# Optimization experiments

Hardware: AMD Instinct MI355X
Metric: run time of the kernel (lower is better)

## Reference

```python
import jax, jax.numpy as jnp
import numpy as np

N_NODES = 50000
N_EDGES = 800000
D_IN, D_HID, D_OUT = 128, 128, 64


def setup_inputs() -> dict:
    key = jax.random.key(0)
    ks = jax.random.split(key, 10)
    return {
        "x": jax.random.normal(ks[0], (N_NODES, D_IN), dtype=jnp.float32),
        "edge_row": jax.random.randint(ks[1], (N_EDGES,), 0, N_NODES, dtype=jnp.int32),
        "edge_col": jax.random.randint(ks[2], (N_EDGES,), 0, N_NODES, dtype=jnp.int32),
        "edge_val": jax.random.uniform(ks[3], (N_EDGES,), dtype=jnp.float32),
        "W1": jax.random.normal(ks[4], (D_IN, D_HID), dtype=jnp.float32) * (1.0 / np.sqrt(D_HID)),
        "b1": jax.random.normal(ks[5], (D_HID,), dtype=jnp.float32) * (1.0 / np.sqrt(D_HID)),
        "W2": jax.random.normal(ks[6], (D_HID, D_HID), dtype=jnp.float32) * (1.0 / np.sqrt(D_HID)),
        "b2": jax.random.normal(ks[7], (D_HID,), dtype=jnp.float32) * (1.0 / np.sqrt(D_HID)),
        "W3": jax.random.normal(ks[8], (D_HID, D_OUT), dtype=jnp.float32) * (1.0 / np.sqrt(D_OUT)),
        "b3": jax.random.normal(ks[9], (D_OUT,), dtype=jnp.float32) * (1.0 / np.sqrt(D_OUT)),
    }


def _gcn_layer(x, edge_row, edge_col, edge_val, W, b):
    # support = x @ W          : dense GEMM [N, d_out]
    support = x @ W
    # spmm(adj, support)[i] = sum_e with row[e]==i: val[e] * support[col[e]]
    gathered = support[edge_col] * edge_val[:, None]  # [E, d_out]
    agg = jax.ops.segment_sum(gathered, edge_row, num_segments=x.shape[0])
    return agg + b


def reference(x, edge_row, edge_col, edge_val, W1, b1, W2, b2, W3, b3):
    # Layer 1 + ReLU (dropout is identity in eval)
    h = jax.nn.relu(_gcn_layer(x, edge_row, edge_col, edge_val, W1, b1))
    # Layer 2 + ReLU
    h = jax.nn.relu(_gcn_layer(h, edge_row, edge_col, edge_val, W2, b2))
    # Layer 3 (no activation)
    return _gcn_layer(h, edge_row, edge_col, edge_val, W3, b3)
```

## Files before the change

### kernel.cpp

```cpp
#include <hip/hip_runtime.h>

#define N_NODES 50000
#define N_EDGES 800000
#define SCAN_TILE 2048
#define CNT_STRIDE 16
#define GEMM1_BLOCKS 768
#define FUSED_BLOCKS 512
#define HIST_BLOCKS ((N_EDGES + 255) / 256)

static_assert(N_NODES < 65536, "col must fit in 16 bits for packed CSR");

typedef __attribute__((ext_vector_type(4))) float f32x4;
typedef __attribute__((ext_vector_type(8))) short bf16x8;

__device__ inline unsigned short f32_to_bf16(float f) {
    unsigned int u = __builtin_bit_cast(unsigned int, f);
    u += 0x7FFF + ((u >> 16) & 1);
    return (unsigned short)(u >> 16);
}
__device__ inline float bf16_to_f32(unsigned short h) {
    unsigned int u = ((unsigned int)h) << 16;
    return __builtin_bit_cast(float, u);
}

#define W128  (128 * 128)
#define W64   (128 * 64)
#define CNT4  (N_NODES * CNT_STRIDE / 4)

__global__ void zero_cnt(int* __restrict__ cnt) {
    int i = blockIdx.x * blockDim.x + threadIdx.x;
    if (i < CNT4) {
        int4 z = {0, 0, 0, 0};
        reinterpret_cast<int4*>(cnt)[i] = z;
    }
}

__global__ void hist_wt(const int* __restrict__ erow, int* __restrict__ cnt,
                        int* __restrict__ rank, const float* __restrict__ W1,
                        const float* __restrict__ W2, const float* __restrict__ W3,
                        unsigned short* __restrict__ Wt1,
                        unsigned short* __restrict__ Wt2,
                        unsigned short* __restrict__ Wt3) {
    if (blockIdx.x < HIST_BLOCKS) {
        int e = blockIdx.x * blockDim.x + threadIdx.x;
        if (e < N_EDGES) rank[e] = atomicAdd(&cnt[(size_t)erow[e] * CNT_STRIDE], 1);
        return;
    }
    long long r = (long long)(blockIdx.x - HIST_BLOCKS) * blockDim.x + threadIdx.x;
    if (r < W128) {
        int k = (int)r / 128, m = (int)r % 128;
        Wt1[m * 128 + k] = f32_to_bf16(W1[r]);
        return;
    }
    r -= W128;
    if (r < W128) {
        int k = (int)r / 128, m = (int)r % 128;
        Wt2[m * 128 + k] = f32_to_bf16(W2[r]);
        return;
    }
    r -= W128;
    if (r < W64) {
        int k = (int)r / 64, m = (int)r % 64;
        Wt3[m * 128 + k] = f32_to_bf16(W3[r]);
    }
}

__global__ void scan_fused(const int* __restrict__ cnt, int* __restrict__ tsum,
                           int* __restrict__ done, int* __restrict__ rptr,
                           int n, int ntiles) {
    __shared__ int sums[256];
    __shared__ int off_s;
    const int t = threadIdx.x;
    const int b = blockIdx.x;
    const int base = b * SCAN_TILE + t * 8;
    int v[8], pref[8];
    int s = 0;
#pragma unroll
    for (int i = 0; i < 8; ++i) {
        v[i] = (base + i < n) ? cnt[(size_t)(base + i) * CNT_STRIDE] : 0;
        s += v[i];
    }
    sums[t] = s;
    __syncthreads();
    for (int off = 1; off < 256; off <<= 1) {
        int x = (t >= off) ? sums[t - off] : 0;
        __syncthreads();
        sums[t] += x;
        __syncthreads();
    }
    int run = sums[t] - s;
#pragma unroll
    for (int i = 0; i < 8; ++i) {
        pref[i] = run;
        run += v[i];
    }
    if (t == 255) {
        tsum[b] = run;
        __threadfence();
        atomicAdd(done, 1);
    }
    if (t == 0) {
        while (__hip_atomic_load(done, __ATOMIC_ACQUIRE, __HIP_MEMORY_SCOPE_AGENT) <
               ntiles) {
        }
        __threadfence();
        int off = 0;
        for (int i = 0; i < b; ++i) off += tsum[i];
        off_s = off;
        if (b == 0) {
            int tot = 0;
            for (int i = 0; i < ntiles; ++i) tot += tsum[i];
            rptr[n] = tot;
        }
    }
    __syncthreads();
    const int off = off_s;
#pragma unroll
    for (int i = 0; i < 8; ++i) {
        int idx = base + i;
        if (idx < n) rptr[idx] = pref[i] + off;
    }
}

template <int NOUT>
__device__ __forceinline__ void mfma_phase(const unsigned short* Xs,
                                           const unsigned short* Ws,
                                           unsigned short* __restrict__ Yb,
                                           int block_row, int N) {
    constexpr int KP = 128 + 8;
    constexpr int NT = NOUT / 16;
    const int tid = threadIdx.x;
    const int wave = tid >> 6;
    const int lane = tid & 63;
    const int m = lane & 15;
    const int quad = lane >> 4;
    const int rowbase = wave * 16;

    f32x4 acc[NT];
#pragma unroll
    for (int t = 0; t < NT; ++t) acc[t] = (f32x4){0.f, 0.f, 0.f, 0.f};

#pragma unroll
    for (int kt = 0; kt < 4; ++kt) {
        bf16x8 a = *reinterpret_cast<const bf16x8*>(
            Xs + (rowbase + m) * KP + kt * 32 + quad * 8);
#pragma unroll
        for (int t = 0; t < NT; ++t) {
            bf16x8 b = *reinterpret_cast<const bf16x8*>(
                Ws + (t * 16 + m) * KP + kt * 32 + quad * 8);
            acc[t] = __builtin_amdgcn_mfma_f32_16x16x32_bf16(a, b, acc[t], 0, 0, 0);
        }
    }

#pragma unroll
    for (int t = 0; t < NT; ++t) {
#pragma unroll
        for (int r = 0; r < 4; ++r) {
            int grow = block_row + rowbase + quad * 4 + r;
            if (grow < N)
                Yb[(size_t)grow * NOUT + t * 16 + m] = f32_to_bf16(acc[t][r]);
        }
    }
}

template <int NOUT>
__device__ __forceinline__ void mfma_phase512(const unsigned short* Xs,
                                              const unsigned short* Ws,
                                              unsigned short* __restrict__ Yb,
                                              int block_row, int N) {
    constexpr int KP = 128 + 8;
    constexpr int NT = NOUT / 16;
    constexpr int NTH = NT / 2;
    const int tid = threadIdx.x;
    const int wave = tid >> 6;
    const int lane = tid & 63;
    const int m = lane & 15;
    const int quad = lane >> 4;
    const int rowbase = (wave & 3) * 16;
    const int tbase = (wave >> 2) * NTH;

    f32x4 acc[NTH];
#pragma unroll
    for (int t = 0; t < NTH; ++t) acc[t] = (f32x4){0.f, 0.f, 0.f, 0.f};

#pragma unroll
    for (int kt = 0; kt < 4; ++kt) {
        bf16x8 a = *reinterpret_cast<const bf16x8*>(
            Xs + (rowbase + m) * KP + kt * 32 + quad * 8);
#pragma unroll
        for (int t = 0; t < NTH; ++t) {
            bf16x8 b = *reinterpret_cast<const bf16x8*>(
                Ws + ((tbase + t) * 16 + m) * KP + kt * 32 + quad * 8);
            acc[t] = __builtin_amdgcn_mfma_f32_16x16x32_bf16(a, b, acc[t], 0, 0, 0);
        }
    }

#pragma unroll
    for (int t = 0; t < NTH; ++t) {
#pragma unroll
        for (int r = 0; r < 4; ++r) {
            int grow = block_row + rowbase + quad * 4 + r;
            if (grow < N)
                Yb[(size_t)grow * NOUT + (tbase + t) * 16 + m] = f32_to_bf16(acc[t][r]);
        }
    }
}

__global__ __launch_bounds__(256) void gemm1_fill(
    const float* __restrict__ x, const unsigned short* __restrict__ Wt,
    unsigned short* __restrict__ Yb, int N, int ntiles,
    const int* __restrict__ erow, const int* __restrict__ ecol,
    const float* __restrict__ eval, const int* __restrict__ rptr,
    const int* __restrict__ rank, unsigned int* __restrict__ cpack) {
    constexpr int KP = 128 + 8;
    __shared__ unsigned short Xs[64 * KP];
    __shared__ unsigned short Ws[128 * KP];
    const int tid = threadIdx.x;

    if (blockIdx.x >= GEMM1_BLOCKS) {
        int e = (blockIdx.x - GEMM1_BLOCKS) * blockDim.x + tid;
        if (e < N_EDGES) {
            int slot = rptr[erow[e]] + rank[e];
            unsigned int p = (unsigned int)(ecol[e] & 0xFFFF) |
                             ((unsigned int)f32_to_bf16(eval[e]) << 16);
            cpack[slot] = p;
        }
        return;
    }

    for (int idx = tid; idx < 128 * 16; idx += 256) {
        int r = idx >> 4, ch = idx & 15;
        uint4 v = *reinterpret_cast<const uint4*>(Wt + r * 128 + ch * 8);
        *reinterpret_cast<uint4*>(Ws + r * KP + ch * 8) = v;
    }

    for (int tile = blockIdx.x; tile < ntiles; tile += GEMM1_BLOCKS) {
        const int block_row = tile * 64;
        for (int idx = tid; idx < 64 * 16; idx += 256) {
            int r = idx >> 4, ch = idx & 15;
            int gr = block_row + r;
            if (gr >= N) gr = N - 1;
            const float4* xp =
                reinterpret_cast<const float4*>(x + (size_t)gr * 128 + ch * 8);
            float4 a = xp[0], b = xp[1];
            uint4 o;
            o.x = (unsigned int)f32_to_bf16(a.x) | ((unsigned int)f32_to_bf16(a.y) << 16);
            o.y = (unsigned int)f32_to_bf16(a.z) | ((unsigned int)f32_to_bf16(a.w) << 16);
            o.z = (unsigned int)f32_to_bf16(b.x) | ((unsigned int)f32_to_bf16(b.y) << 16);
            o.w = (unsigned int)f32_to_bf16(b.z) | ((unsigned int)f32_to_bf16(b.w) << 16);
            *reinterpret_cast<uint4*>(Xs + r * KP + ch * 8) = o;
        }
        __syncthreads();
        mfma_phase<128>(Xs, Ws, Yb, block_row, N);
        __syncthreads();
    }
}

template <int NOUT>
__global__ __launch_bounds__(512, 4) void gemm_fused_agg(
    const unsigned short* __restrict__ S,
    const int* __restrict__ rptr, const unsigned int* __restrict__ cpack,
    const float* __restrict__ bias,
    const unsigned short* __restrict__ Wt,
    unsigned short* __restrict__ Yb,
    int N, int ntiles) {
    constexpr int KP = 128 + 8;
    __shared__ unsigned short Xs[64 * KP];
    __shared__ unsigned short Ws[NOUT * KP];
    const int tid = threadIdx.x;
    const int group = tid >> 4;
    const int f8 = tid & 15;

    for (int idx = tid; idx < NOUT * 16; idx += 512) {
        int r = idx >> 4, ch = idx & 15;
        uint4 v = *reinterpret_cast<const uint4*>(Wt + r * 128 + ch * 8);
        *reinterpret_cast<uint4*>(Ws + r * KP + ch * 8) = v;
    }

    float bv[8];
#pragma unroll
    for (int i = 0; i < 8; ++i) bv[i] = bias[f8 * 8 + i];

    for (int tile = blockIdx.x; tile < ntiles; tile += gridDim.x) {
        const int block_row = tile * 64;
#pragma unroll
        for (int r4 = 0; r4 < 2; ++r4) {
            const int row = r4 * 32 + group;
            const int node = block_row + row;
            float acc[8];
#pragma unroll
            for (int i = 0; i < 8; ++i) acc[i] = bv[i];
            if (node < N) {
                const int beg = rptr[node];
                const int end = rptr[node + 1];
                int j = beg;
                for (; j + 8 <= end; j += 8) {
                    unsigned int p[8];
                    uint4 s[8];
#pragma unroll
                    for (int u = 0; u < 8; ++u) p[u] = cpack[j + u];
#pragma unroll
                    for (int u = 0; u < 8; ++u)
                        s[u] = *reinterpret_cast<const uint4*>(
                            S + (size_t)(p[u] & 0xFFFF) * 128 + f8 * 8);
#pragma unroll
                    for (int u = 0; u < 8; ++u) {
                        const float v = bf16_to_f32((unsigned short)(p[u] >> 16));
                        const unsigned short* sp =
                            reinterpret_cast<const unsigned short*>(&s[u]);
#pragma unroll
                        for (int i = 0; i < 8; ++i)
                            acc[i] = fmaf(v, bf16_to_f32(sp[i]), acc[i]);
                    }
                }
                if (j + 4 <= end) {
                    unsigned int p[4];
                    uint4 s[4];
#pragma unroll
                    for (int u = 0; u < 4; ++u) p[u] = cpack[j + u];
#pragma unroll
                    for (int u = 0; u < 4; ++u)
                        s[u] = *reinterpret_cast<const uint4*>(
                            S + (size_t)(p[u] & 0xFFFF) * 128 + f8 * 8);
#pragma unroll
                    for (int u = 0; u < 4; ++u) {
                        const float v = bf16_to_f32((unsigned short)(p[u] >> 16));
                        const unsigned short* sp =
                            reinterpret_cast<const unsigned short*>(&s[u]);
#pragma unroll
                        for (int i = 0; i < 8; ++i)
                            acc[i] = fmaf(v, bf16_to_f32(sp[i]), acc[i]);
                    }
                    j += 4;
                }
                if (j + 2 <= end) {
                    unsigned int p[2];
                    uint4 s[2];
#pragma unroll
                    for (int u = 0; u < 2; ++u) p[u] = cpack[j + u];
#pragma unroll
                    for (int u = 0; u < 2; ++u)
                        s[u] = *reinterpret_cast<const uint4*>(
                            S + (size_t)(p[u] & 0xFFFF) * 128 + f8 * 8);
#pragma unroll
                    for (int u = 0; u < 2; ++u) {
                        const float v = bf16_to_f32((unsigned short)(p[u] >> 16));
                        const unsigned short* sp =
                            reinterpret_cast<const unsigned short*>(&s[u]);
#pragma unroll
                        for (int i = 0; i < 8; ++i)
                            acc[i] = fmaf(v, bf16_to_f32(sp[i]), acc[i]);
                    }
                    j += 2;
                }
                if (j < end) {
                    unsigned int p = cpack[j];
                    uint4 s = *reinterpret_cast<const uint4*>(
                        S + (size_t)(p & 0xFFFF) * 128 + f8 * 8);
                    const float v = bf16_to_f32((unsigned short)(p >> 16));
                    const unsigned short* sp =
                        reinterpret_cast<const unsigned short*>(&s);
#pragma unroll
                    for (int i = 0; i < 8; ++i)
                        acc[i] = fmaf(v, bf16_to_f32(sp[i]), acc[i]);
                }
            }
            uint4 o;
            o.x = (unsigned int)f32_to_bf16(fmaxf(acc[0], 0.f)) |
                  ((unsigned int)f32_to_bf16(fmaxf(acc[1], 0.f)) << 16);
            o.y = (unsigned int)f32_to_bf16(fmaxf(acc[2], 0.f)) |
                  ((unsigned int)f32_to_bf16(fmaxf(acc[3], 0.f)) << 16);
            o.z = (unsigned int)f32_to_bf16(fmaxf(acc[4], 0.f)) |
                  ((unsigned int)f32_to_bf16(fmaxf(acc[5], 0.f)) << 16);
            o.w = (unsigned int)f32_to_bf16(fmaxf(acc[6], 0.f)) |
                  ((unsigned int)f32_to_bf16(fmaxf(acc[7], 0.f)) << 16);
            *reinterpret_cast<uint4*>(Xs + row * KP + f8 * 8) = o;
        }
        __syncthreads();
        mfma_phase512<NOUT>(Xs, Ws, Yb, block_row, N);
        __syncthreads();
    }
}

__global__ void aggregate_bf16_64(const unsigned short* __restrict__ S,
                                  const int* __restrict__ rptr,
                                  const unsigned int* __restrict__ cpack,
                                  const float* __restrict__ bias,
                                  float* __restrict__ out, int N) {
    const int node = blockIdx.x * (blockDim.x / 16) + threadIdx.x / 16;
    const int f4 = threadIdx.x & 15;
    if (node >= N) return;
    const int beg = rptr[node];
    const int end = rptr[node + 1];
    float acc[4];
#pragma unroll
    for (int i = 0; i < 4; ++i) acc[i] = bias[f4 * 4 + i];
    int j = beg;
    for (; j + 8 <= end; j += 8) {
        unsigned int p[8];
        uint2 s[8];
#pragma unroll
        for (int u = 0; u < 8; ++u) p[u] = cpack[j + u];
#pragma unroll
        for (int u = 0; u < 8; ++u)
            s[u] = *reinterpret_cast<const uint2*>(S + (size_t)(p[u] & 0xFFFF) * 64 + f4 * 4);
#pragma unroll
        for (int u = 0; u < 8; ++u) {
            const float v = bf16_to_f32((unsigned short)(p[u] >> 16));
            const unsigned short* sp = reinterpret_cast<const unsigned short*>(&s[u]);
#pragma unroll
            for (int i = 0; i < 4; ++i) acc[i] = fmaf(v, bf16_to_f32(sp[i]), acc[i]);
        }
    }
    if (j + 4 <= end) {
        unsigned int p[4];
        uint2 s[4];
#pragma unroll
        for (int u = 0; u < 4; ++u) p[u] = cpack[j + u];
#pragma unroll
        for (int u = 0; u < 4; ++u)
            s[u] = *reinterpret_cast<const uint2*>(S + (size_t)(p[u] & 0xFFFF) * 64 + f4 * 4);
#pragma unroll
        for (int u = 0; u < 4; ++u) {
            const float v = bf16_to_f32((unsigned short)(p[u] >> 16));
            const unsigned short* sp = reinterpret_cast<const unsigned short*>(&s[u]);
#pragma unroll
            for (int i = 0; i < 4; ++i) acc[i] = fmaf(v, bf16_to_f32(sp[i]), acc[i]);
        }
        j += 4;
    }
    if (j + 2 <= end) {
        unsigned int p[2];
        uint2 s[2];
#pragma unroll
        for (int u = 0; u < 2; ++u) p[u] = cpack[j + u];
#pragma unroll
        for (int u = 0; u < 2; ++u)
            s[u] = *reinterpret_cast<const uint2*>(S + (size_t)(p[u] & 0xFFFF) * 64 + f4 * 4);
#pragma unroll
        for (int u = 0; u < 2; ++u) {
            const float v = bf16_to_f32((unsigned short)(p[u] >> 16));
            const unsigned short* sp = reinterpret_cast<const unsigned short*>(&s[u]);
#pragma unroll
            for (int i = 0; i < 4; ++i) acc[i] = fmaf(v, bf16_to_f32(sp[i]), acc[i]);
        }
        j += 2;
    }
    if (j < end) {
        unsigned int p = cpack[j];
        uint2 s = *reinterpret_cast<const uint2*>(S + (size_t)(p & 0xFFFF) * 64 + f4 * 4);
        const float v = bf16_to_f32((unsigned short)(p >> 16));
        const unsigned short* sp = reinterpret_cast<const unsigned short*>(&s);
#pragma unroll
        for (int i = 0; i < 4; ++i) acc[i] = fmaf(v, bf16_to_f32(sp[i]), acc[i]);
    }
    float4 o = {acc[0], acc[1], acc[2], acc[3]};
    *reinterpret_cast<float4*>(out + (size_t)node * 64 + f4 * 4) = o;
}

extern "C" void kernel_launch(void* const* d_in, const int* in_sizes, int n_in,
                              void* d_out, int out_size, void* d_ws, size_t ws_size,
                              hipStream_t stream) {
    const float* x    = (const float*)d_in[0];
    const int*   erow = (const int*)d_in[1];
    const int*   ecol = (const int*)d_in[2];
    const float* eval = (const float*)d_in[3];
    const float* W1   = (const float*)d_in[4];
    const float* b1   = (const float*)d_in[5];
    const float* W2   = (const float*)d_in[6];
    const float* b2   = (const float*)d_in[7];
    const float* W3   = (const float*)d_in[8];
    const float* b3   = (const float*)d_in[9];
    float* out = (float*)d_out;

    const size_t nf = (size_t)N_NODES * 128;
    unsigned short* SA  = (unsigned short*)d_ws;
    unsigned short* SB  = SA + nf;
    unsigned short* Wt1 = SB + nf;
    unsigned short* Wt2 = Wt1 + 128 * 128;
    unsigned short* Wt3 = Wt2 + 128 * 128;
    int*   cnt    = (int*)(Wt3 + 64 * 128);
    int*   rank   = cnt + (size_t)N_NODES * CNT_STRIDE;
    int*   rptr   = rank + N_EDGES;
    unsigned int* cpack = (unsigned int*)(rptr + N_NODES + 1);
    int*   stsum  = (int*)(cpack + N_EDGES);
    int*   done   = cnt + 1;

    const int blk = 256;
    const int ntiles_g = (N_NODES + 63) / 64;
    const int agg_grid = (int)(((long long)N_NODES * 16 + blk - 1) / blk);
    const int ntiles = (N_NODES + SCAN_TILE - 1) / SCAN_TILE;
    const int wt_blocks = (W128 + W128 + W64 + blk - 1) / blk;

    zero_cnt<<<(CNT4 + blk - 1) / blk, blk, 0, stream>>>(cnt);
    hist_wt<<<HIST_BLOCKS + wt_blocks, blk, 0, stream>>>(erow, cnt, rank, W1, W2, W3,
                                                         Wt1, Wt2, Wt3);
    scan_fused<<<ntiles, 256, 0, stream>>>(cnt, stsum, done, rptr, N_NODES, ntiles);

    gemm1_fill<<<GEMM1_BLOCKS + HIST_BLOCKS, 256, 0, stream>>>(
        x, Wt1, SA, N_NODES, ntiles_g, erow, ecol, eval, rptr, rank, cpack);

    gemm_fused_agg<128><<<FUSED_BLOCKS, 512, 0, stream>>>(
        SA, rptr, cpack, b1, Wt2, SB, N_NODES, ntiles_g);

    gemm_fused_agg<64><<<FUSED_BLOCKS, 512, 0, stream>>>(
        SB, rptr, cpack, b2, Wt3, SA, N_NODES, ntiles_g);

    aggregate_bf16_64<<<agg_grid, blk, 0, stream>>>(SA, rptr, cpack, b3, out, N_NODES);
}
```

Baseline: 233.3 us.

## Overlap edge histogram with layer-1 GEMM and move CSR fill to own kernel

Merges the count-zeroing and weight transpose/convert into one prep kernel, then runs the edge histogram (atomic rank assignment) in the same launch as the layer-1 GEMM instead of in a separate kernel. The CSR packing step, which previously shared a launch with the GEMM, becomes its own small kernel after the scan. The launch count stays the same, but the GEMM now overlaps the atomic-heavy histogram rather than the lighter scatter fill. A risk is that the atomics contend with the GEMM's memory traffic.

```diff
diff --git a/kernel.cpp b/kernel.cpp
--- a/kernel.cpp
+++ b/kernel.cpp
@@ -27,26 +27,18 @@
 #define W64   (128 * 64)
 #define CNT4  (N_NODES * CNT_STRIDE / 4)
 
-__global__ void zero_cnt(int* __restrict__ cnt) {
-    int i = blockIdx.x * blockDim.x + threadIdx.x;
-    if (i < CNT4) {
+__global__ void prep(int* __restrict__ cnt, const float* __restrict__ W1,
+                     const float* __restrict__ W2, const float* __restrict__ W3,
+                     unsigned short* __restrict__ Wt1,
+                     unsigned short* __restrict__ Wt2,
+                     unsigned short* __restrict__ Wt3) {
+    long long r = (long long)blockIdx.x * blockDim.x + threadIdx.x;
+    if (r < CNT4) {
         int4 z = {0, 0, 0, 0};
-        reinterpret_cast<int4*>(cnt)[i] = z;
-    }
-}
-
-__global__ void hist_wt(const int* __restrict__ erow, int* __restrict__ cnt,
-                        int* __restrict__ rank, const float* __restrict__ W1,
-                        const float* __restrict__ W2, const float* __restrict__ W3,
-                        unsigned short* __restrict__ Wt1,
-                        unsigned short* __restrict__ Wt2,
-                        unsigned short* __restrict__ Wt3) {
-    if (blockIdx.x < HIST_BLOCKS) {
-        int e = blockIdx.x * blockDim.x + threadIdx.x;
-        if (e < N_EDGES) rank[e] = atomicAdd(&cnt[(size_t)erow[e] * CNT_STRIDE], 1);
+        reinterpret_cast<int4*>(cnt)[r] = z;
         return;
     }
-    long long r = (long long)(blockIdx.x - HIST_BLOCKS) * blockDim.x + threadIdx.x;
+    r -= CNT4;
     if (r < W128) {
         int k = (int)r / 128, m = (int)r % 128;
         Wt1[m * 128 + k] = f32_to_bf16(W1[r]);
@@ -62,63 +54,6 @@
     if (r < W64) {
         int k = (int)r / 64, m = (int)r % 64;
         Wt3[m * 128 + k] = f32_to_bf16(W3[r]);
-    }
-}
-
-__global__ void scan_fused(const int* __restrict__ cnt, int* __restrict__ tsum,
-                           int* __restrict__ done, int* __restrict__ rptr,
-                           int n, int ntiles) {
-    __shared__ int sums[256];
-    __shared__ int off_s;
-    const int t = threadIdx.x;
-    const int b = blockIdx.x;
-    const int base = b * SCAN_TILE + t * 8;
-    int v[8], pref[8];
-    int s = 0;
-#pragma unroll
-    for (int i = 0; i < 8; ++i) {
-        v[i] = (base + i < n) ? cnt[(size_t)(base + i) * CNT_STRIDE] : 0;
-        s += v[i];
-    }
-    sums[t] = s;
-    __syncthreads();
-    for (int off = 1; off < 256; off <<= 1) {
-        int x = (t >= off) ? sums[t - off] : 0;
-        __syncthreads();
-        sums[t] += x;
-        __syncthreads();
-    }
-    int run = sums[t] - s;
-#pragma unroll
-    for (int i = 0; i < 8; ++i) {
-        pref[i] = run;
-        run += v[i];
-    }
-    if (t == 255) {
-        tsum[b] = run;
-        __threadfence();
-        atomicAdd(done, 1);
-    }
-    if (t == 0) {
-        while (__hip_atomic_load(done, __ATOMIC_ACQUIRE, __HIP_MEMORY_SCOPE_AGENT) <
-               ntiles) {
-        }
-        __threadfence();
-        int off = 0;
-        for (int i = 0; i < b; ++i) off += tsum[i];
-        off_s = off;
-        if (b == 0) {
-            int tot = 0;
-            for (int i = 0; i < ntiles; ++i) tot += tsum[i];
-            rptr[n] = tot;
-        }
-    }
-    __syncthreads();
-    const int off = off_s;
-#pragma unroll
-    for (int i = 0; i < 8; ++i) {
-        int idx = base + i;
-        if (idx < n) rptr[idx] = pref[i] + off;
     }
 }
 
@@ -161,6 +96,118 @@
                 Yb[(size_t)grow * NOUT + t * 16 + m] = f32_to_bf16(acc[t][r]);
         }
     }
+}
+
+__global__ __launch_bounds__(256) void gemm1_hist(
+    const float* __restrict__ x, const unsigned short* __restrict__ Wt,
+    unsigned short* __restrict__ Yb, int N, int ntiles,
+    const int* __restrict__ erow, int* __restrict__ cnt, int* __restrict__ rank) {
+    constexpr int KP = 128 + 8;
+    __shared__ unsigned short Xs[64 * KP];
+    __shared__ unsigned short Ws[128 * KP];
+    const int tid = threadIdx.x;
+
+    if (blockIdx.x >= GEMM1_BLOCKS) {
+        int e = (blockIdx.x - GEMM1_BLOCKS) * blockDim.x + tid;
+        if (e < N_EDGES) rank[e] = atomicAdd(&cnt[(size_t)erow[e] * CNT_STRIDE], 1);
+        return;
+    }
+
+    for (int idx = tid; idx < 128 * 16; idx += 256) {
+        int r = idx >> 4, ch = idx & 15;
+        uint4 v = *reinterpret_cast<const uint4*>(Wt + r * 128 + ch * 8);
+        *reinterpret_cast<uint4*>(Ws + r * KP + ch * 8) = v;
+    }
+
+    for (int tile = blockIdx.x; tile < ntiles; tile += GEMM1_BLOCKS) {
+        const int block_row = tile * 64;
+        for (int idx = tid; idx < 64 * 16; idx += 256) {
+            int r = idx >> 4, ch = idx & 15;
+            int gr = block_row + r;
+            if (gr >= N) gr = N - 1;
+            const float4* xp =
+                reinterpret_cast<const float4*>(x + (size_t)gr * 128 + ch * 8);
+            float4 a = xp[0], b = xp[1];
+            uint4 o;
+            o.x = (unsigned int)f32_to_bf16(a.x) | ((unsigned int)f32_to_bf16(a.y) << 16);
+            o.y = (unsigned int)f32_to_bf16(a.z) | ((unsigned int)f32_to_bf16(a.w) << 16);
+            o.z = (unsigned int)f32_to_bf16(b.x) | ((unsigned int)f32_to_bf16(b.y) << 16);
+            o.w = (unsigned int)f32_to_bf16(b.z) | ((unsigned int)f32_to_bf16(b.w) << 16);
+            *reinterpret_cast<uint4*>(Xs + r * KP + ch * 8) = o;
+        }
+        __syncthreads();
+        mfma_phase<128>(Xs, Ws, Yb, block_row, N);
+        __syncthreads();
+    }
+}
+
+__global__ void scan_fused(const int* __restrict__ cnt, int* __restrict__ tsum,
+                           int* __restrict__ done, int* __restrict__ rptr,
+                           int n, int ntiles) {
+    __shared__ int sums[256];
+    __shared__ int off_s;
+    const int t = threadIdx.x;
+    const int b = blockIdx.x;
+    const int base = b * SCAN_TILE + t * 8;
+    int v[8], pref[8];
+    int s = 0;
+#pragma unroll
+    for (int i = 0; i < 8; ++i) {
+        v[i] = (base + i < n) ? cnt[(size_t)(base + i) * CNT_STRIDE] : 0;
+        s += v[i];
+    }
+    sums[t] = s;
+    __syncthreads();
+    for (int off = 1; off < 256; off <<= 1) {
+        int x = (t >= off) ? sums[t - off] : 0;
+        __syncthreads();
+        sums[t] += x;
+        __syncthreads();
+    }
+    int run = sums[t] - s;
+#pragma unroll
+    for (int i = 0; i < 8; ++i) {
+        pref[i] = run;
+        run += v[i];
+    }
+    if (t == 255) {
+        tsum[b] = run;
+        __threadfence();
+        atomicAdd(done, 1);
+    }
+    if (t == 0) {
+        while (__hip_atomic_load(done, __ATOMIC_ACQUIRE, __HIP_MEMORY_SCOPE_AGENT) <
+               ntiles) {
+        }
+        __threadfence();
+        int off = 0;
+        for (int i = 0; i < b; ++i) off += tsum[i];
+        off_s = off;
+        if (b == 0) {
+            int tot = 0;
+            for (int i = 0; i < ntiles; ++i) tot += tsum[i];
+            rptr[n] = tot;
+        }
+    }
+    __syncthreads();
+    const int off = off_s;
+#pragma unroll
+    for (int i = 0; i < 8; ++i) {
+        int idx = base + i;
+        if (idx < n) rptr[idx] = pref[i] + off;
+    }
+}
+
+__global__ void fill_csr(const int* __restrict__ erow, const int* __restrict__ ecol,
+                         const float* __restrict__ eval, const int* __restrict__ rptr,
+                         const int* __restrict__ rank,
+                         unsigned int* __restrict__ cpack) {
+    int e = blockIdx.x * blockDim.x + threadIdx.x;
+    if (e >= N_EDGES) return;
+    int slot = rptr[erow[e]] + rank[e];
+    unsigned int p = (unsigned int)(ecol[e] & 0xFFFF) |
+                     ((unsigned int)f32_to_bf16(eval[e]) << 16);
+    cpack[slot] = p;
 }
 
 template <int NOUT>
@@ -206,56 +253,6 @@
     }
 }
 
-__global__ __launch_bounds__(256) void gemm1_fill(
-    const float* __restrict__ x, const unsigned short* __restrict__ Wt,
-    unsigned short* __restrict__ Yb, int N, int ntiles,
-    const int* __restrict__ erow, const int* __restrict__ ecol,
-    const float* __restrict__ eval, const int* __restrict__ rptr,
-    const int* __restrict__ rank, unsigned int* __restrict__ cpack) {
-    constexpr int KP = 128 + 8;
-    __shared__ unsigned short Xs[64 * KP];
-    __shared__ unsigned short Ws[128 * KP];
-    const int tid = threadIdx.x;
-
-    if (blockIdx.x >= GEMM1_BLOCKS) {
-        int e = (blockIdx.x - GEMM1_BLOCKS) * blockDim.x + tid;
-        if (e < N_EDGES) {
-            int slot = rptr[erow[e]] + rank[e];
-            unsigned int p = (unsigned int)(ecol[e] & 0xFFFF) |
-                             ((unsigned int)f32_to_bf16(eval[e]) << 16);
-            cpack[slot] = p;
-        }
-        return;
-    }
-
-    for (int idx = tid; idx < 128 * 16; idx += 256) {
-        int r = idx >> 4, ch = idx & 15;
-        uint4 v = *reinterpret_cast<const uint4*>(Wt + r * 128 + ch * 8);
-        *reinterpret_cast<uint4*>(Ws + r * KP + ch * 8) = v;
-    }
-
-    for (int tile = blockIdx.x; tile < ntiles; tile += GEMM1_BLOCKS) {
-        const int block_row = tile * 64;
-        for (int idx = tid; idx < 64 * 16; idx += 256) {
-            int r = idx >> 4, ch = idx & 15;
-            int gr = block_row + r;
-            if (gr >= N) gr = N - 1;
-            const float4* xp =
-                reinterpret_cast<const float4*>(x + (size_t)gr * 128 + ch * 8);
-            float4 a = xp[0], b = xp[1];
-            uint4 o;
-            o.x = (unsigned int)f32_to_bf16(a.x) | ((unsigned int)f32_to_bf16(a.y) << 16);
-            o.y = (unsigned int)f32_to_bf16(a.z) | ((unsigned int)f32_to_bf16(a.w) << 16);
-            o.z = (unsigned int)f32_to_bf16(b.x) | ((unsigned int)f32_to_bf16(b.y) << 16);
-            o.w = (unsigned int)f32_to_bf16(b.z) | ((unsigned int)f32_to_bf16(b.w) << 16);
-            *reinterpret_cast<uint4*>(Xs + r * KP + ch * 8) = o;
-        }
-        __syncthreads();
-        mfma_phase<128>(Xs, Ws, Yb, block_row, N);
-        __syncthreads();
-    }
-}
-
 template <int NOUT>
 __global__ __launch_bounds__(512, 4) void gemm_fused_agg(
     const unsigned short* __restrict__ S,
@@ -490,15 +487,19 @@
     const int ntiles_g = (N_NODES + 63) / 64;
     const int agg_grid = (int)(((long long)N_NODES * 16 + blk - 1) / blk);
     const int ntiles = (N_NODES + SCAN_TILE - 1) / SCAN_TILE;
-    const int wt_blocks = (W128 + W128 + W64 + blk - 1) / blk;
-
-    zero_cnt<<<(CNT4 + blk - 1) / blk, blk, 0, stream>>>(cnt);
-    hist_wt<<<HIST_BLOCKS + wt_blocks, blk, 0, stream>>>(erow, cnt, rank, W1, W2, W3,
-                                                         Wt1, Wt2, Wt3);
+
+    {
+        long long total = (long long)CNT4 + W128 + W128 + W64;
+        prep<<<(int)((total + blk - 1) / blk), blk, 0, stream>>>(
+            cnt, W1, W2, W3, Wt1, Wt2, Wt3);
+    }
+
+    gemm1_hist<<<GEMM1_BLOCKS + HIST_BLOCKS, 256, 0, stream>>>(
+        x, Wt1, SA, N_NODES, ntiles_g, erow, cnt, rank);
+
     scan_fused<<<ntiles, 256, 0, stream>>>(cnt, stsum, done, rptr, N_NODES, ntiles);
 
-    gemm1_fill<<<GEMM1_BLOCKS + HIST_BLOCKS, 256, 0, stream>>>(
-        x, Wt1, SA, N_NODES, ntiles_g, erow, ecol, eval, rptr, rank, cpack);
+    fill_csr<<<HIST_BLOCKS, blk, 0, stream>>>(erow, ecol, eval, rptr, rank, cpack);
 
     gemm_fused_agg<128><<<FUSED_BLOCKS, 512, 0, stream>>>(
         SA, rptr, cpack, b1, Wt2, SB, N_NODES, ntiles_g);
```

New measurement: 235.3 us. About the same (+0.8%).
